# Performance work log

Hardware: AMD Instinct MI355X
Metric: run time of the kernel (lower is better)

## Reference

```python
import jax, jax.numpy as jnp
import numpy as np

B, K, M, D = 8, 4096, 4096, 512
L = K + M  # output length along axis -2
MASK_INIT_STD = 0.01  # jax.nn.initializers.normal() default stddev


def setup_inputs() -> dict:
    key = jax.random.key(0)
    k1, k2, k3 = jax.random.split(key, 3)
    inputs = jax.random.normal(k1, (B, K, D), dtype=jnp.float32)
    mask_embedding = jax.random.normal(k2, (D,), dtype=jnp.float32) * MASK_INIT_STD
    # Per-batch permutations of [0, L) so keep/fill indices partition the output.
    perm = jax.vmap(lambda k: jax.random.permutation(k, L))(jax.random.split(k3, B))
    keep_position_ids = perm[:, :K].astype(jnp.int32)
    mask_position_ids = perm[:, K:].astype(jnp.int32)
    return {
        "inputs": inputs,
        "mask_position_ids": mask_position_ids,
        "keep_position_ids": keep_position_ids,
        "mask_embedding": mask_embedding,
        "axis": -2,
    }


def reference(inputs, mask_position_ids, keep_position_ids, mask_embedding, axis):
    # Faithful math of MaskFiller with keep_position_ids given (fill_by_scatter):
    # out[b, keep_ids[b, k], :] = inputs[b, k, :]
    # out[b, mask_ids[b, m], :] = mask_embedding
    # The original implements this as one-hot dot_generals; a true scatter is the
    # same math without the O(L*K) blow-up.
    assert axis == -2
    b, k, d = inputs.shape
    m = mask_position_ids.shape[-1]
    length = k + m
    bidx = jnp.arange(b)[:, None]
    out = jnp.zeros((b, length, d), dtype=inputs.dtype)
    out = out.at[bidx, keep_position_ids].set(inputs)
    upd = jnp.broadcast_to(mask_embedding.astype(inputs.dtype), (b, m, d))
    out = out.at[bidx, mask_position_ids].set(upd)
    return out
```

## Files before the change

kernel.cpp:

```cpp
#include <hip/hip_runtime.h>
#include <hip/hip_bf16.h>


constexpr int B = 8;
constexpr int K = 4096;
constexpr int M = 4096;
constexpr int L = K + M;
constexpr int D = 512;
constexpr int D4 = D / 4;

__global__ __launch_bounds__(128)
void MaskFiller_scatter_kernel(const float4* __restrict__ inputs,
                               const int* __restrict__ mask_ids,
                               const int* __restrict__ keep_ids,
                               const float4* __restrict__ emb,
                               float4* __restrict__ out) {
    const int row = blockIdx.x;
    const int b   = row / L;
    const int r   = row - b * L;
    const int d4  = threadIdx.x;

    float4 v;
    int dst;
    if (r < K) {
        dst = keep_ids[b * K + r];
        v   = inputs[(size_t)(b * K + r) * D4 + d4];
    } else {
        const int m = r - K;
        dst = mask_ids[b * M + m];
        v   = emb[d4];
    }
    out[((size_t)b * L + dst) * D4 + d4] = v;
}

extern "C" void kernel_launch(void* const* d_in, const int* in_sizes, int n_in,
                              void* d_out, int out_size, void* d_ws, size_t ws_size,
                              hipStream_t stream) {
    const float4* inputs   = (const float4*)d_in[0];
    const int*    mask_ids = (const int*)d_in[1];
    const int*    keep_ids = (const int*)d_in[2];
    const float4* emb      = (const float4*)d_in[3];
    float4* out = (float4*)d_out;

    dim3 grid(B * L);
    dim3 block(128);
    MaskFiller_scatter_kernel<<<grid, block, 0, stream>>>(inputs, mask_ids, keep_ids, emb, out);
}
```

Measured before the change: 186.3 us.

## Use persistent grid-stride waves copying two rows each with nontemporal stores

```diff
diff --git a/kernel.cpp b/kernel.cpp
--- a/kernel.cpp
+++ b/kernel.cpp
@@ -1,36 +1,63 @@
 #include <hip/hip_runtime.h>
-#include <hip/hip_bf16.h>
 
 
-constexpr int B = 8;
-constexpr int K = 4096;
-constexpr int M = 4096;
-constexpr int L = K + M;
-constexpr int D = 512;
+constexpr int B  = 8;
+constexpr int K  = 4096;
+constexpr int M  = 4096;
+constexpr int L  = K + M;
+constexpr int D  = 512;
 constexpr int D4 = D / 4;
 
-__global__ __launch_bounds__(128)
-void MaskFiller_scatter_kernel(const float4* __restrict__ inputs,
-                               const int* __restrict__ mask_ids,
-                               const int* __restrict__ keep_ids,
-                               const float4* __restrict__ emb,
-                               float4* __restrict__ out) {
-    const int row = blockIdx.x;
-    const int b   = row / L;
-    const int r   = row - b * L;
-    const int d4  = threadIdx.x;
+typedef float f32x4 __attribute__((ext_vector_type(4)));
 
-    float4 v;
-    int dst;
-    if (r < K) {
-        dst = keep_ids[b * K + r];
-        v   = inputs[(size_t)(b * K + r) * D4 + d4];
-    } else {
-        const int m = r - K;
-        dst = mask_ids[b * M + m];
-        v   = emb[d4];
+__device__ __forceinline__ void nt_store(float4* p, const float4& v) {
+    __builtin_nontemporal_store(*(const f32x4*)&v, (f32x4*)p);
+}
+
+__global__ __launch_bounds__(256)
+void MaskFiller_scatter_v2(const float4* __restrict__ inputs,
+                           const int* __restrict__ mask_ids,
+                           const int* __restrict__ keep_ids,
+                           const float4* __restrict__ emb,
+                           float4* __restrict__ out) {
+    const int lane  = threadIdx.x & 63;
+    const int wid   = blockIdx.x * (256 / 64) + (threadIdx.x >> 6);
+    const int nwave = gridDim.x * (256 / 64);
+
+    const float4 e0 = emb[lane];
+    const float4 e1 = emb[lane + 64];
+
+    for (int base = wid * 2; base < B * K; base += nwave * 2) {
+        const int r0 = base;
+        const int r1 = base + 1;
+        const int dst0 = keep_ids[r0];
+        const int dst1 = keep_ids[r1];
+        const float4* s0 = inputs + (size_t)r0 * D4;
+        const float4* s1 = inputs + (size_t)r1 * D4;
+        const float4 a0 = s0[lane];
+        const float4 a1 = s0[lane + 64];
+        const float4 a2 = s1[lane];
+        const float4 a3 = s1[lane + 64];
+        float4* o0 = out + ((size_t)(r0 >> 12) * L + dst0) * D4;
+        float4* o1 = out + ((size_t)(r1 >> 12) * L + dst1) * D4;
+        nt_store(o0 + lane,      a0);
+        nt_store(o0 + lane + 64, a1);
+        nt_store(o1 + lane,      a2);
+        nt_store(o1 + lane + 64, a3);
     }
-    out[((size_t)b * L + dst) * D4 + d4] = v;
+
+    for (int base = wid * 2; base < B * M; base += nwave * 2) {
+        const int m0 = base;
+        const int m1 = base + 1;
+        const int dst0 = mask_ids[m0];
+        const int dst1 = mask_ids[m1];
+        float4* o0 = out + ((size_t)(m0 >> 12) * L + dst0) * D4;
+        float4* o1 = out + ((size_t)(m1 >> 12) * L + dst1) * D4;
+        nt_store(o0 + lane,      e0);
+        nt_store(o0 + lane + 64, e1);
+        nt_store(o1 + lane,      e0);
+        nt_store(o1 + lane + 64, e1);
+    }
 }
 
 extern "C" void kernel_launch(void* const* d_in, const int* in_sizes, int n_in,
@@ -42,7 +69,7 @@
     const float4* emb      = (const float4*)d_in[3];
     float4* out = (float4*)d_out;
 
-    dim3 grid(B * L);
-    dim3 block(128);
-    MaskFiller_scatter_kernel<<<grid, block, 0, stream>>>(inputs, mask_ids, keep_ids, emb, out);
+    dim3 grid(2048);
+    dim3 block(256);
+    MaskFiller_scatter_v2<<<grid, block, 0, stream>>>(inputs, mask_ids, keep_ids, emb, out);
 }
```

Result: no change. 188.9 us (+1.4%).
